# Kernel optimization log

Hardware: AMD Instinct MI355X
Metric: run time of the kernel (lower is better)

## Reference

```python
import jax, jax.numpy as jnp
import numpy as np


def setup_inputs() -> dict:
    key = jax.random.key(0)
    ks = jax.random.split(key, 7)
    B, H, W = 32, 28, 28
    C3, C4 = 1024, 2048
    C = C3 + C4            # 3072
    L1 = 9                 # num_landmarks + 1
    A, NC = 312, 200
    return {
        "l3": jax.random.normal(ks[0], (B, C3, H, W), jnp.float32),
        "l4": jax.random.normal(ks[1], (B, C4, H // 2, W // 2), jnp.float32),
        "conv_w": jax.random.normal(ks[2], (L1, C), jnp.float32) * 0.02,
        "modulation": jnp.ones((1, C, L1), jnp.float32),
        "attr_w": jax.random.normal(ks[3], (A, C), jnp.float32) * 0.02,
        "attr_b": jnp.zeros((A,), jnp.float32),
        "class_w": jax.random.normal(ks[4], (NC, A), jnp.float32) * 0.02,
    }


def reference(l3, l4, conv_w, modulation, attr_w, attr_b, class_w):
    b, c3, h, w = l3.shape
    # F.interpolate(l4, (h, w), mode='bilinear', align_corners=False)
    l4_up = jax.image.resize(l4, (b, l4.shape[1], h, w), method="bilinear")
    x = jnp.concatenate([l4_up, l3], axis=1)            # (b, 3072, h, w)

    # 1x1 conv: ab[b,l,h,w] = sum_c w[l,c] * x[b,c,h,w]
    ab = jnp.einsum("lc,bchw->blhw", conv_w, x)
    b_sq = jnp.sum(x * x, axis=1, keepdims=True)        # (b,1,h,w)
    a_sq = jnp.sum(conv_w, axis=1)[None, :, None, None]  # (1,L+1,1,1)  (matches torch: weight.sum(1), NOT squared)
    maps = jax.nn.softmax(-(b_sq - 2.0 * ab + a_sq), axis=1)  # Softmax2d = softmax over channels

    # (maps[:,None] * x[:,:,None]).mean((-1,-2))  ->  batched GEMM over spatial dim
    all_features = jnp.einsum("blhw,bchw->bcl", maps, x) / (h * w)  # (b, c, L+1)

    mod = all_features * modulation                     # dropout is identity at eval
    # permute(0,2,1)[:, :-1, :].mean(1) == mean over landmark dim excluding background
    mean_features = jnp.mean(mod[:, :, :-1], axis=2)    # (b, c)

    attr_scores = mean_features @ attr_w.T + attr_b      # (b, 312)
    class_scores = attr_scores @ class_w.T               # (b, 200)
    return attr_scores, class_scores, maps, all_features
```

## Files before the change

kernel.cpp:

```cpp
#include <hip/hip_runtime.h>
#include <math.h>

#define B_    32
#define C3_   1024
#define C4_   2048
#define C_    3072
#define P_    784
#define Q_    196
#define L_    9
#define NG_   25088
#define A_    312
#define NC_   200

#define ATTR_OFF  0
#define CLASS_OFF 9984
#define MAPS_OFF  16384
#define AF_OFF    242176

#define ASQ_OFF   0
#define MF_OFF    16
#define PART3_OFF 98320
#define PAF_OFF   98320
#define Y4P_OFF   (PART3_OFF + 16 * 9 * NG_)
#define LOGITS_OFF Y4P_OFF
#define Y_OFF     (Y4P_OFF + 32 * 32 * 9 * Q_)
#define MP_OFF    (Y_OFF + 32 * 9 * Q_)

typedef __attribute__((ext_vector_type(8))) short bf16x8;
typedef __attribute__((ext_vector_type(4))) float f32x4;

__device__ __forceinline__ short f2bf(float f) {
    union { float f; unsigned u; } v; v.f = f;
    unsigned r = v.u + 0x7FFFu + ((v.u >> 16) & 1u);
    return (short)(r >> 16);
}

__global__ __launch_bounds__(256, 4) void kA(
        const float* __restrict__ l3, const float* __restrict__ l4,
        const float* __restrict__ conv_w,
        float* __restrict__ part3, float* __restrict__ y4p) {
    int bid = blockIdx.x;
    int t = threadIdx.x;

    const float* xp;
    float* outp;
    int xpitch, opitch, cbase_w;
    if (bid < 400) {
        int slab = bid / 25, rb = bid % 25;
        int tid2 = rb * 256 + t;
        if (tid2 >= 6272) return;
        int b = tid2 / 196, px = (tid2 % 196) * 4;
        xp = l3 + ((size_t)b * C3_ + slab * 64) * P_ + px;
        xpitch = P_;
        cbase_w = C4_ + slab * 64;
        outp = part3 + (size_t)(slab * 9) * NG_ + b * P_ + px;
        opitch = NG_;
    } else {
        int idx = bid - 400;
        int grp = idx / 7, rb = idx % 7;
        int tid2 = rb * 256 + t;
        if (tid2 >= 1568) return;
        int b = tid2 / 49, q = (tid2 % 49) * 4;
        xp = l4 + ((size_t)b * C4_ + grp * 64) * Q_ + q;
        xpitch = Q_;
        cbase_w = grp * 64;
        outp = y4p + ((size_t)(b * 32 + grp) * 9) * Q_ + q;
        opitch = Q_;
    }

    float acc[9][4];
#pragma unroll
    for (int l = 0; l < 9; ++l)
#pragma unroll
        for (int j = 0; j < 4; ++j) acc[l][j] = 0.f;

    float4 v[2][8];
#pragma unroll
    for (int k = 0; k < 8; ++k)
        v[0][k] = *(const float4*)(xp + (size_t)k * xpitch);

#pragma unroll
    for (int c = 0; c < 64; c += 8) {
        int cur = (c >> 3) & 1, nxt = cur ^ 1;
        if (c < 56) {
#pragma unroll
            for (int k = 0; k < 8; ++k)
                v[nxt][k] = *(const float4*)(xp + (size_t)(c + 8 + k) * xpitch);
        }
#pragma unroll
        for (int l = 0; l < 9; ++l) {
            const float4 w0 = *(const float4*)(conv_w + l * C_ + cbase_w + c);
            const float4 w1 = *(const float4*)(conv_w + l * C_ + cbase_w + c + 4);
            const float wv[8] = {w0.x, w0.y, w0.z, w0.w, w1.x, w1.y, w1.z, w1.w};
#pragma unroll
            for (int k = 0; k < 8; ++k) {
                acc[l][0] = fmaf(wv[k], v[cur][k].x, acc[l][0]);
                acc[l][1] = fmaf(wv[k], v[cur][k].y, acc[l][1]);
                acc[l][2] = fmaf(wv[k], v[cur][k].z, acc[l][2]);
                acc[l][3] = fmaf(wv[k], v[cur][k].w, acc[l][3]);
            }
        }
    }
#pragma unroll
    for (int l = 0; l < 9; ++l)
        *(float4*)(outp + (size_t)l * opitch) =
            make_float4(acc[l][0], acc[l][1], acc[l][2], acc[l][3]);
}

__global__ __launch_bounds__(256) void kB(const float* __restrict__ y4p,
                                          const float* __restrict__ conv_w,
                                          float* __restrict__ Y,
                                          float* __restrict__ asq) {
    if (blockIdx.x == 221) {
        __shared__ float red[256];
        int t = threadIdx.x;
        for (int l = 0; l < L_; ++l) {
            float s = 0.f;
            for (int c = t; c < C_; c += 256) s += conv_w[l * C_ + c];
            red[t] = s; __syncthreads();
            for (int o = 128; o > 0; o >>= 1) {
                if (t < o) red[t] += red[t + o];
                __syncthreads();
            }
            if (t == 0) asq[l] = red[0];
            __syncthreads();
        }
        return;
    }
    int tid = blockIdx.x * 256 + threadIdx.x;
    if (tid >= 32 * 9 * Q_) return;
    int b = tid / (9 * Q_);
    int r = tid % (9 * Q_);
    float s = 0.f;
#pragma unroll
    for (int grp = 0; grp < 32; ++grp)
        s += y4p[(size_t)(b * 32 + grp) * (9 * Q_) + r];
    Y[(size_t)b * (9 * Q_) + r] = s;
}

__global__ __launch_bounds__(256) void kC1(const float* __restrict__ part3,
                                           const float* __restrict__ Y,
                                           const float* __restrict__ asq,
                                           float* __restrict__ logits) {
    int idx = blockIdx.x * 256 + threadIdx.x;
    int l = idx / NG_, g = idx % NG_;
    int b = g / P_, p = g % P_;
    int yy = p / 28, xx = p % 28;
    float sy = 0.5f * yy - 0.25f, sx = 0.5f * xx - 0.25f;
    float fyf = floorf(sy), fxf = floorf(sx);
    float fy = sy - fyf, fx = sx - fxf;
    int ya = max(0, (int)fyf), yb = min(13, (int)fyf + 1);
    int xa = max(0, (int)fxf), xb = min(13, (int)fxf + 1);
    float w00 = (1.f - fy) * (1.f - fx), w01 = (1.f - fy) * fx;
    float w10 = fy * (1.f - fx),         w11 = fy * fx;
    const float* Yl = Y + ((size_t)b * 9 + l) * Q_;
    float ab4 = w00 * Yl[ya * 14 + xa] + w01 * Yl[ya * 14 + xb]
              + w10 * Yl[yb * 14 + xa] + w11 * Yl[yb * 14 + xb];
    float ab3 = 0.f;
#pragma unroll
    for (int sl = 0; sl < 16; ++sl)
        ab3 += part3[(size_t)(sl * 9 + l) * NG_ + g];
    logits[idx] = 2.f * (ab4 + ab3) - asq[l];
}

__global__ __launch_bounds__(256) void kC2(const float* __restrict__ logits,
                                           float* __restrict__ out_maps) {
    int g = blockIdx.x * 256 + threadIdx.x;
    int b = g / P_, p = g % P_;
    float v[9];
#pragma unroll
    for (int l = 0; l < 9; ++l) v[l] = logits[(size_t)l * NG_ + g];
    float m = v[0];
#pragma unroll
    for (int l = 1; l < 9; ++l) m = fmaxf(m, v[l]);
    float sum = 0.f;
#pragma unroll
    for (int l = 0; l < 9; ++l) { v[l] = expf(v[l] - m); sum += v[l]; }
    float inv = 1.f / sum;
#pragma unroll
    for (int l = 0; l < 9; ++l)
        out_maps[(size_t)b * (L_ * P_) + l * P_ + p] = v[l] * inv;
}

__device__ __forceinline__ int adj_taps(int q, int* ys, float* wy) {
    if (q == 0)  { ys[0] = 0;  wy[0] = 1.00f; ys[1] = 1;  wy[1] = 0.75f;
                   ys[2] = 2;  wy[2] = 0.25f; return 3; }
    if (q == 13) { ys[0] = 25; wy[0] = 0.25f; ys[1] = 26; wy[1] = 0.75f;
                   ys[2] = 27; wy[2] = 1.00f; return 3; }
    ys[0] = 2 * q - 1; wy[0] = 0.25f;
    ys[1] = 2 * q;     wy[1] = 0.75f;
    ys[2] = 2 * q + 1; wy[2] = 0.75f;
    ys[3] = 2 * q + 2; wy[3] = 0.25f;
    return 4;
}

__global__ __launch_bounds__(256) void kD(const float* __restrict__ maps,
                                          float* __restrict__ Mp) {
    int tid = blockIdx.x * 256 + threadIdx.x;
    if (tid >= 32 * 9 * Q_) return;
    int b = tid / (9 * Q_);
    int r = tid % (9 * Q_);
    int l = r / Q_, q = r % Q_;
    int qy = q / 14, qx = q % 14;
    int ys[4], xs[4]; float wy[4], wx[4];
    int ny = adj_taps(qy, ys, wy);
    int nx = adj_taps(qx, xs, wx);
    const float* mrow = maps + (size_t)b * (L_ * P_) + l * P_;
    float s = 0.f;
    for (int i = 0; i < ny; ++i) {
        float rs = 0.f;
        for (int j = 0; j < nx; ++j)
            rs = fmaf(wx[j], mrow[ys[i] * 28 + xs[j]], rs);
        s = fmaf(wy[i], rs, s);
    }
    Mp[(size_t)b * (9 * Q_) + r] = s;
}

#define SA 232
__global__ __launch_bounds__(256) void kE(
        const float* __restrict__ l3, const float* __restrict__ l4,
        const float* __restrict__ maps, const float* __restrict__ Mp,
        float* __restrict__ out_af, float* __restrict__ paf) {
    __shared__ short As[64 * SA];
    __shared__ short Bs[16 * SA];
    int bid = blockIdx.x;
    int t = threadIdx.x;
    int wave = t >> 6, lane = t & 63;
    int row16 = lane & 15, quad = lane >> 4;

    const float* xsrc; size_t xstride;
    const float* bsrc; size_t bstride;
    int b, c0, h;
    bool isl4 = (bid < 1024);
    if (isl4) {
        b = bid >> 5;
        c0 = (bid & 31) * 64;
        h = 0;
        xsrc = l4 + ((size_t)b * C4_ + c0) * Q_;
        xstride = Q_;
        bsrc = Mp + (size_t)b * (9 * Q_);
        bstride = Q_;
    } else {
        int idx = bid - 1024;
        b = idx >> 6;
        c0 = ((idx >> 2) & 15) * 64;
        h = idx & 3;
        xsrc = l3 + ((size_t)b * C3_ + c0) * P_ + h * Q_;
        xstride = P_;
        bsrc = maps + (size_t)b * (L_ * P_) + h * Q_;
        bstride = P_;
    }

    for (int i = t; i < 64 * 49; i += 256) {
        int r = i / 49, j = (i % 49) * 4;
        float4 v = *(const float4*)(xsrc + (size_t)r * xstride + j);
        ushort4 o;
        o.x = (unsigned short)f2bf(v.x); o.y = (unsigned short)f2bf(v.y);
        o.z = (unsigned short)f2bf(v.z); o.w = (unsigned short)f2bf(v.w);
        *(ushort4*)(As + r * SA + j) = o;
    }
    for (int i = t; i < 64 * 9; i += 256) {
        int r = i / 9, j = 196 + (i % 9) * 4;
        *(ushort4*)(As + r * SA + j) = make_ushort4(0, 0, 0, 0);
    }
    for (int i = t; i < 16 * 58; i += 256) {
        int r = i / 58, j = (i % 58) * 4;
        ushort4 o = make_ushort4(0, 0, 0, 0);
        if (r < 9 && j < 196) {
            float4 v = *(const float4*)(bsrc + (size_t)r * bstride + j);
            o.x = (unsigned short)f2bf(v.x); o.y = (unsigned short)f2bf(v.y);
            o.z = (unsigned short)f2bf(v.z); o.w = (unsigned short)f2bf(v.w);
        }
        *(ushort4*)(Bs + r * SA + j) = o;
    }
    __syncthreads();

    const short* arow = As + (wave * 16 + row16) * SA;
    const short* brow = Bs + row16 * SA;
    f32x4 acc = {0.f, 0.f, 0.f, 0.f};
#pragma unroll
    for (int k0 = 0; k0 < 224; k0 += 32) {
        bf16x8 a = *(const bf16x8*)(arow + k0 + quad * 8);
        bf16x8 bv = *(const bf16x8*)(brow + k0 + quad * 8);
        acc = __builtin_amdgcn_mfma_f32_16x16x32_bf16(a, bv, acc, 0, 0, 0);
    }
    int l = row16;
    if (l < 9) {
        int c = c0 + wave * 16 + quad * 4;
        if (isl4) {
            size_t base = ((size_t)b * C_ + c) * 9 + l;
#pragma unroll
            for (int r = 0; r < 4; ++r)
                out_af[base + (size_t)r * 9] = acc[r] * (1.f / 784.f);
        } else {
            size_t base = ((size_t)(h * B_ + b) * C3_ + c) * 9 + l;
#pragma unroll
            for (int r = 0; r < 4; ++r)
                paf[base + (size_t)r * 9] = acc[r];
        }
    }
}

__global__ __launch_bounds__(256) void kMF(const float* __restrict__ paf,
                                           const float* __restrict__ mod,
                                           float* __restrict__ out_af,
                                           float* __restrict__ mf) {
    int i = blockIdx.x * 256 + threadIdx.x;
    if (i >= B_ * C_) return;
    int b = i / C_, c = i % C_;
    float af[9];
    if (c < C4_) {
#pragma unroll
        for (int l = 0; l < 9; ++l) af[l] = out_af[(size_t)i * 9 + l];
    } else {
        int c3 = c - C4_;
#pragma unroll
        for (int l = 0; l < 9; ++l) {
            float s = 0.f;
#pragma unroll
            for (int hh = 0; hh < 4; ++hh)
                s += paf[((size_t)(hh * B_ + b) * C3_ + c3) * 9 + l];
            af[l] = s * (1.f / 784.f);
            out_af[(size_t)i * 9 + l] = af[l];
        }
    }
    const float* m = mod + (size_t)c * 9;
    float s = 0.f;
#pragma unroll
    for (int l = 0; l < 8; ++l) s = fmaf(af[l], m[l], s);
    mf[i] = s * 0.125f;
}

__global__ __launch_bounds__(256) void kF(
        const float* __restrict__ mf, const float* __restrict__ attr_w,
        const float* __restrict__ attr_b, float* __restrict__ out_attr) {
    int idx = blockIdx.x * 4 + (threadIdx.x >> 6);
    int lane = threadIdx.x & 63;
    int b = idx / A_, a = idx % A_;
    const float4* wr = (const float4*)(attr_w + (size_t)a * C_);
    const float4* mr = (const float4*)(mf + (size_t)b * C_);
    float acc = 0.f;
    for (int j = lane; j < C_ / 4; j += 64) {
        float4 w = wr[j], m = mr[j];
        acc += w.x * m.x + w.y * m.y + w.z * m.z + w.w * m.w;
    }
    acc += __shfl_xor(acc, 1);  acc += __shfl_xor(acc, 2);
    acc += __shfl_xor(acc, 4);  acc += __shfl_xor(acc, 8);
    acc += __shfl_xor(acc, 16); acc += __shfl_xor(acc, 32);
    if (lane == 0) out_attr[idx] = acc + attr_b[a];
}

__global__ __launch_bounds__(256) void kG(
        const float* __restrict__ attr, const float* __restrict__ class_w,
        float* __restrict__ out_class) {
    int idx = blockIdx.x * 4 + (threadIdx.x >> 6);
    int lane = threadIdx.x & 63;
    int b = idx / NC_, n = idx % NC_;
    float acc = 0.f;
    for (int a = lane; a < A_; a += 64)
        acc += attr[b * A_ + a] * class_w[n * A_ + a];
    acc += __shfl_xor(acc, 1);  acc += __shfl_xor(acc, 2);
    acc += __shfl_xor(acc, 4);  acc += __shfl_xor(acc, 8);
    acc += __shfl_xor(acc, 16); acc += __shfl_xor(acc, 32);
    if (lane == 0) out_class[idx] = acc;
}

extern "C" void kernel_launch(void* const* d_in, const int* in_sizes, int n_in,
                              void* d_out, int out_size, void* d_ws, size_t ws_size,
                              hipStream_t stream) {
    (void)in_sizes; (void)n_in; (void)out_size; (void)ws_size;
    const float* l3         = (const float*)d_in[0];
    const float* l4         = (const float*)d_in[1];
    const float* conv_w     = (const float*)d_in[2];
    const float* modulation = (const float*)d_in[3];
    const float* attr_w     = (const float*)d_in[4];
    const float* attr_b     = (const float*)d_in[5];
    const float* class_w    = (const float*)d_in[6];
    float* out = (float*)d_out;
    float* ws  = (float*)d_ws;
    float* asq    = ws + ASQ_OFF;
    float* mf     = ws + MF_OFF;
    float* part3  = ws + PART3_OFF;
    float* paf    = ws + PAF_OFF;
    float* y4p    = ws + Y4P_OFF;
    float* logits = ws + LOGITS_OFF;
    float* Y      = ws + Y_OFF;
    float* Mp     = ws + MP_OFF;

    kA<<<624, 256, 0, stream>>>(l3, l4, conv_w, part3, y4p);
    kB<<<222, 256, 0, stream>>>(y4p, conv_w, Y, asq);
    kC1<<<882, 256, 0, stream>>>(part3, Y, asq, logits);
    kC2<<<98, 256, 0, stream>>>(logits, out + MAPS_OFF);
    kD<<<221, 256, 0, stream>>>(out + MAPS_OFF, Mp);
    kE<<<3072, 256, 0, stream>>>(l3, l4, out + MAPS_OFF, Mp, out + AF_OFF, paf);
    kMF<<<384, 256, 0, stream>>>(paf, modulation, out + AF_OFF, mf);
    kF<<<(B_ * A_) / 4, 256, 0, stream>>>(mf, attr_w, attr_b, out + ATTR_OFF);
    kG<<<(B_ * NC_) / 4, 256, 0, stream>>>(out + ATTR_OFF, class_w,
                                           out + CLASS_OFF);
}
```

Measured before the change: 307.9 us.

## Deepen kA load batching, batch kE global loads, and keep attr weights in registers in kF

kA now double-buffers 16 channels per stage instead of 8 and relaxes its launch bound to 2 blocks per SM, which raises memory-level parallelism at the cost of more registers. kE issues all global float4 loads for its A and B tiles before doing any bf16 conversion or shared-memory stores, so load latency overlaps. kF is restructured so each wave loads one attr_w row into registers once and reuses it across all 32 batches, which cuts redundant weight reads but launches only 78 blocks.

```diff
diff --git a/kernel.cpp b/kernel.cpp
--- a/kernel.cpp
+++ b/kernel.cpp
@@ -35,7 +35,7 @@
     return (short)(r >> 16);
 }
 
-__global__ __launch_bounds__(256, 4) void kA(
+__global__ __launch_bounds__(256, 2) void kA(
         const float* __restrict__ l3, const float* __restrict__ l4,
         const float* __restrict__ conv_w,
         float* __restrict__ part3, float* __restrict__ y4p) {
@@ -74,26 +74,30 @@
 #pragma unroll
         for (int j = 0; j < 4; ++j) acc[l][j] = 0.f;
 
-    float4 v[2][8];
-#pragma unroll
-    for (int k = 0; k < 8; ++k)
+    float4 v[2][16];
+#pragma unroll
+    for (int k = 0; k < 16; ++k)
         v[0][k] = *(const float4*)(xp + (size_t)k * xpitch);
 
 #pragma unroll
-    for (int c = 0; c < 64; c += 8) {
-        int cur = (c >> 3) & 1, nxt = cur ^ 1;
-        if (c < 56) {
-#pragma unroll
-            for (int k = 0; k < 8; ++k)
-                v[nxt][k] = *(const float4*)(xp + (size_t)(c + 8 + k) * xpitch);
+    for (int g = 0; g < 4; ++g) {
+        int cur = g & 1, nxt = cur ^ 1;
+        if (g < 3) {
+#pragma unroll
+            for (int k = 0; k < 16; ++k)
+                v[nxt][k] = *(const float4*)(xp + (size_t)((g + 1) * 16 + k) * xpitch);
         }
 #pragma unroll
         for (int l = 0; l < 9; ++l) {
-            const float4 w0 = *(const float4*)(conv_w + l * C_ + cbase_w + c);
-            const float4 w1 = *(const float4*)(conv_w + l * C_ + cbase_w + c + 4);
-            const float wv[8] = {w0.x, w0.y, w0.z, w0.w, w1.x, w1.y, w1.z, w1.w};
-#pragma unroll
-            for (int k = 0; k < 8; ++k) {
+            const float* wp = conv_w + l * C_ + cbase_w + g * 16;
+            const float4 w0 = *(const float4*)(wp);
+            const float4 w1 = *(const float4*)(wp + 4);
+            const float4 w2 = *(const float4*)(wp + 8);
+            const float4 w3 = *(const float4*)(wp + 12);
+            const float wv[16] = {w0.x, w0.y, w0.z, w0.w, w1.x, w1.y, w1.z, w1.w,
+                                  w2.x, w2.y, w2.z, w2.w, w3.x, w3.y, w3.z, w3.w};
+#pragma unroll
+            for (int k = 0; k < 16; ++k) {
                 acc[l][0] = fmaf(wv[k], v[cur][k].x, acc[l][0]);
                 acc[l][1] = fmaf(wv[k], v[cur][k].y, acc[l][1]);
                 acc[l][2] = fmaf(wv[k], v[cur][k].z, acc[l][2]);
@@ -217,7 +221,7 @@
 }
 
 #define SA 232
-__global__ __launch_bounds__(256) void kE(
+__global__ __launch_bounds__(256, 4) void kE(
         const float* __restrict__ l3, const float* __restrict__ l4,
         const float* __restrict__ maps, const float* __restrict__ Mp,
         float* __restrict__ out_af, float* __restrict__ paf) {
@@ -251,27 +255,55 @@
         bstride = P_;
     }
 
-    for (int i = t; i < 64 * 49; i += 256) {
-        int r = i / 49, j = (i % 49) * 4;
-        float4 v = *(const float4*)(xsrc + (size_t)r * xstride + j);
-        ushort4 o;
-        o.x = (unsigned short)f2bf(v.x); o.y = (unsigned short)f2bf(v.y);
-        o.z = (unsigned short)f2bf(v.z); o.w = (unsigned short)f2bf(v.w);
-        *(ushort4*)(As + r * SA + j) = o;
-    }
-    for (int i = t; i < 64 * 9; i += 256) {
-        int r = i / 9, j = 196 + (i % 9) * 4;
-        *(ushort4*)(As + r * SA + j) = make_ushort4(0, 0, 0, 0);
-    }
-    for (int i = t; i < 16 * 58; i += 256) {
-        int r = i / 58, j = (i % 58) * 4;
-        ushort4 o = make_ushort4(0, 0, 0, 0);
-        if (r < 9 && j < 196) {
-            float4 v = *(const float4*)(bsrc + (size_t)r * bstride + j);
-            o.x = (unsigned short)f2bf(v.x); o.y = (unsigned short)f2bf(v.y);
-            o.z = (unsigned short)f2bf(v.z); o.w = (unsigned short)f2bf(v.w);
-        }
-        *(ushort4*)(Bs + r * SA + j) = o;
+    float4 va[13];
+#pragma unroll
+    for (int u = 0; u < 13; ++u) {
+        int i = u * 256 + t;
+        if (i < 64 * 49) {
+            int r = i / 49, j = (i % 49) * 4;
+            va[u] = *(const float4*)(xsrc + (size_t)r * xstride + j);
+        }
+    }
+    float4 vb[4];
+#pragma unroll
+    for (int u = 0; u < 4; ++u) {
+        int i = u * 256 + t;
+        if (i < 16 * 58) {
+            int r = i / 58, j = (i % 58) * 4;
+            vb[u] = make_float4(0.f, 0.f, 0.f, 0.f);
+            if (r < 9 && j < 196)
+                vb[u] = *(const float4*)(bsrc + (size_t)r * bstride + j);
+        }
+    }
+#pragma unroll
+    for (int u = 0; u < 13; ++u) {
+        int i = u * 256 + t;
+        if (i < 64 * 49) {
+            int r = i / 49, j = (i % 49) * 4;
+            ushort4 o;
+            o.x = (unsigned short)f2bf(va[u].x); o.y = (unsigned short)f2bf(va[u].y);
+            o.z = (unsigned short)f2bf(va[u].z); o.w = (unsigned short)f2bf(va[u].w);
+            *(ushort4*)(As + r * SA + j) = o;
+        }
+    }
+#pragma unroll
+    for (int u = 0; u < 3; ++u) {
+        int i = u * 256 + t;
+        if (i < 64 * 9) {
+            int r = i / 9, j = 196 + (i % 9) * 4;
+            *(ushort4*)(As + r * SA + j) = make_ushort4(0, 0, 0, 0);
+        }
+    }
+#pragma unroll
+    for (int u = 0; u < 4; ++u) {
+        int i = u * 256 + t;
+        if (i < 16 * 58) {
+            int r = i / 58, j = (i % 58) * 4;
+            ushort4 o;
+            o.x = (unsigned short)f2bf(vb[u].x); o.y = (unsigned short)f2bf(vb[u].y);
+            o.z = (unsigned short)f2bf(vb[u].z); o.w = (unsigned short)f2bf(vb[u].w);
+            *(ushort4*)(Bs + r * SA + j) = o;
+        }
     }
     __syncthreads();
 
@@ -331,23 +363,30 @@
     mf[i] = s * 0.125f;
 }
 
-__global__ __launch_bounds__(256) void kF(
+__global__ __launch_bounds__(256, 2) void kF(
         const float* __restrict__ mf, const float* __restrict__ attr_w,
         const float* __restrict__ attr_b, float* __restrict__ out_attr) {
-    int idx = blockIdx.x * 4 + (threadIdx.x >> 6);
+    int a = blockIdx.x * 4 + (threadIdx.x >> 6);
     int lane = threadIdx.x & 63;
-    int b = idx / A_, a = idx % A_;
-    const float4* wr = (const float4*)(attr_w + (size_t)a * C_);
-    const float4* mr = (const float4*)(mf + (size_t)b * C_);
-    float acc = 0.f;
-    for (int j = lane; j < C_ / 4; j += 64) {
-        float4 w = wr[j], m = mr[j];
-        acc += w.x * m.x + w.y * m.y + w.z * m.z + w.w * m.w;
-    }
-    acc += __shfl_xor(acc, 1);  acc += __shfl_xor(acc, 2);
-    acc += __shfl_xor(acc, 4);  acc += __shfl_xor(acc, 8);
-    acc += __shfl_xor(acc, 16); acc += __shfl_xor(acc, 32);
-    if (lane == 0) out_attr[idx] = acc + attr_b[a];
+    const float* wr = attr_w + (size_t)a * C_;
+    float4 w[12];
+#pragma unroll
+    for (int j = 0; j < 12; ++j)
+        w[j] = *(const float4*)(wr + j * 256 + lane * 4);
+    float bias = attr_b[a];
+    for (int b = 0; b < B_; ++b) {
+        const float* mr = mf + (size_t)b * C_;
+        float acc = 0.f;
+#pragma unroll
+        for (int j = 0; j < 12; ++j) {
+            float4 m = *(const float4*)(mr + j * 256 + lane * 4);
+            acc += w[j].x * m.x + w[j].y * m.y + w[j].z * m.z + w[j].w * m.w;
+        }
+        acc += __shfl_xor(acc, 1);  acc += __shfl_xor(acc, 2);
+        acc += __shfl_xor(acc, 4);  acc += __shfl_xor(acc, 8);
+        acc += __shfl_xor(acc, 16); acc += __shfl_xor(acc, 32);
+        if (lane == 0) out_attr[b * A_ + a] = acc + bias;
+    }
 }
 
 __global__ __launch_bounds__(256) void kG(
@@ -394,7 +433,7 @@
     kD<<<221, 256, 0, stream>>>(out + MAPS_OFF, Mp);
     kE<<<3072, 256, 0, stream>>>(l3, l4, out + MAPS_OFF, Mp, out + AF_OFF, paf);
     kMF<<<384, 256, 0, stream>>>(paf, modulation, out + AF_OFF, mf);
-    kF<<<(B_ * A_) / 4, 256, 0, stream>>>(mf, attr_w, attr_b, out + ATTR_OFF);
+    kF<<<78, 256, 0, stream>>>(mf, attr_w, attr_b, out + ATTR_OFF);
     kG<<<(B_ * NC_) / 4, 256, 0, stream>>>(out + ATTR_OFF, class_w,
                                            out + CLASS_OFF);
 }
```

Measured after the change: 337.8 us. 1.1x slower.
